# Optimization experiments

Hardware: AMD Instinct MI355X
Metric: run time of the kernel (lower is better)

## Reference

```python
import jax, jax.numpy as jnp
import numpy as np

B, MUL = 512, 64
DIMS = {0: 1, 1: 3, 2: 5}
PAIRS = [(0, 0), (0, 1), (0, 2), (1, 1), (1, 2), (2, 2)]  # l2 >= l1 (filter_symmetric)
LS_OUT = (0, 1, 2)


def _triples():
    for l1, l2 in PAIRS:
        for l3 in range(abs(l1 - l2), l1 + l2 + 1):
            if l3 in LS_OUT:
                yield (l1, l2, l3)


def setup_inputs() -> dict:
    key = jax.random.key(0)
    inp = {}
    for l in LS_OUT:
        key, k = jax.random.split(key)
        inp['x%d' % l] = jax.random.normal(k, (B, MUL, DIMS[l]), dtype=jnp.float32)
    for (l1, l2, l3) in _triples():
        key, k = jax.random.split(key)
        inp['w3j_%d_%d_%d' % (l1, l2, l3)] = jax.random.normal(
            k, (DIMS[l1], DIMS[l2], DIMS[l3]), dtype=jnp.float32) * 0.1
    return inp


def _forward(x, w):
    # ls_rule='full', channel_rule='full', filter_symmetric=True
    out = {l3: [] for l3 in LS_OUT}
    for l1, l2 in PAIRS:
        # outer product over channels and m-components: [B, i*j, 2l1+1, 2l2+1]
        op = jnp.einsum('bim,bjn->bijmn', x[l1], x[l2])
        b, i, j, m, n = op.shape
        op = op.reshape(b, i * j, m, n)
        for l3 in range(abs(l1 - l2), l1 + l2 + 1):
            if l3 in LS_OUT:
                # contract with Clebsch-Gordan / w3j coefficients
                out[l3].append(jnp.einsum('mnM,bimn->biM', w[(l1, l2, l3)], op))
    return tuple(jnp.concatenate(out[l3], axis=1) for l3 in LS_OUT)


def reference(x0, x1, x2,
              w3j_0_0_0, w3j_0_1_1, w3j_0_2_2,
              w3j_1_1_0, w3j_1_1_1, w3j_1_1_2,
              w3j_1_2_1, w3j_1_2_2,
              w3j_2_2_0, w3j_2_2_1, w3j_2_2_2):
    x = {0: x0, 1: x1, 2: x2}
    w = {(0, 0, 0): w3j_0_0_0, (0, 1, 1): w3j_0_1_1, (0, 2, 2): w3j_0_2_2,
         (1, 1, 0): w3j_1_1_0, (1, 1, 1): w3j_1_1_1, (1, 1, 2): w3j_1_1_2,
         (1, 2, 1): w3j_1_2_1, (1, 2, 2): w3j_1_2_2,
         (2, 2, 0): w3j_2_2_0, (2, 2, 1): w3j_2_2_1, (2, 2, 2): w3j_2_2_2}
    return _forward(x, w)
```

## Files before the change

kernel.cpp:

```cpp
#include <hip/hip_runtime.h>


#define OUT1_BASE (512 * 12288)
#define OUT2_BASE (OUT1_BASE + 512 * 49152)

#define WO_000 0
#define WO_011 1
#define WO_022 10
#define WO_110 35
#define WO_111 44
#define WO_112 71
#define WO_121 116
#define WO_122 161
#define WO_220 236
#define WO_221 261
#define WO_222 336
#define W_TOTAL 461

__global__ __launch_bounds__(256) void tp_kernel(
    const float* __restrict__ x0, const float* __restrict__ x1, const float* __restrict__ x2,
    const float* __restrict__ w000, const float* __restrict__ w011, const float* __restrict__ w022,
    const float* __restrict__ w110, const float* __restrict__ w111, const float* __restrict__ w112,
    const float* __restrict__ w121, const float* __restrict__ w122,
    const float* __restrict__ w220, const float* __restrict__ w221, const float* __restrict__ w222,
    float* __restrict__ out)
{
    __shared__ float s_x0[64];
    __shared__ float s_x1[192];
    __shared__ float s_x2[320];
    __shared__ float s_w[W_TOTAL];

    const int b    = blockIdx.x >> 4;
    const int tile = blockIdx.x & 15;
    const int t    = threadIdx.x;

    if (t < 64)  s_x0[t] = x0[b * 64 + t];
    if (t < 192) s_x1[t] = x1[b * 192 + t];
#pragma unroll
    for (int idx = t; idx < 320; idx += 256) s_x2[idx] = x2[b * 320 + idx];

    if (t < 1)   s_w[WO_000 + t] = w000[t];
    if (t < 9)   s_w[WO_011 + t] = w011[t];
    if (t < 25)  s_w[WO_022 + t] = w022[t];
    if (t < 9)   s_w[WO_110 + t] = w110[t];
    if (t < 27)  s_w[WO_111 + t] = w111[t];
    if (t < 45)  s_w[WO_112 + t] = w112[t];
    if (t < 45)  s_w[WO_121 + t] = w121[t];
    if (t < 75)  s_w[WO_122 + t] = w122[t];
    if (t < 25)  s_w[WO_220 + t] = w220[t];
    if (t < 75)  s_w[WO_221 + t] = w221[t];
    if (t < 125) s_w[WO_222 + t] = w222[t];

    __syncthreads();

    const int c = tile * 256 + t;
    const int i = c >> 6;
    const int j = c & 63;

    const float a0 = s_x0[i];
    const float b0 = s_x0[j];
    float a1m[3], b1n[3], a2m[5], b2n[5];
#pragma unroll
    for (int m = 0; m < 3; ++m) a1m[m] = s_x1[i * 3 + m];
#pragma unroll
    for (int n = 0; n < 3; ++n) b1n[n] = s_x1[j * 3 + n];
#pragma unroll
    for (int m = 0; m < 5; ++m) a2m[m] = s_x2[i * 5 + m];
#pragma unroll
    for (int n = 0; n < 5; ++n) b2n[n] = s_x2[j * 5 + n];

    float* __restrict__ out0 = out + (size_t)b * 12288;
    float* __restrict__ out1 = out + OUT1_BASE + (size_t)b * 49152;
    float* __restrict__ out2 = out + OUT2_BASE + (size_t)b * 81920;

    out0[c] = s_w[WO_000] * (a0 * b0);

    {
        float o[3] = {0.f, 0.f, 0.f};
#pragma unroll
        for (int n = 0; n < 3; ++n) {
            const float p = a0 * b1n[n];
#pragma unroll
            for (int M = 0; M < 3; ++M) o[M] += s_w[WO_011 + n * 3 + M] * p;
        }
        float* op = out1 + (size_t)c * 3;
#pragma unroll
        for (int M = 0; M < 3; ++M) op[M] = o[M];
    }

    {
        float o[5] = {0.f, 0.f, 0.f, 0.f, 0.f};
#pragma unroll
        for (int n = 0; n < 5; ++n) {
            const float p = a0 * b2n[n];
#pragma unroll
            for (int M = 0; M < 5; ++M) o[M] += s_w[WO_022 + n * 5 + M] * p;
        }
        float* op = out2 + (size_t)c * 5;
#pragma unroll
        for (int M = 0; M < 5; ++M) op[M] = o[M];
    }

    {
        float p[9];
#pragma unroll
        for (int m = 0; m < 3; ++m)
#pragma unroll
            for (int n = 0; n < 3; ++n) p[m * 3 + n] = a1m[m] * b1n[n];

        {
            float o = 0.f;
#pragma unroll
            for (int k = 0; k < 9; ++k) o += s_w[WO_110 + k] * p[k];
            out0[4096 + c] = o;
        }
        {
            float o[3] = {0.f, 0.f, 0.f};
#pragma unroll
            for (int k = 0; k < 9; ++k)
#pragma unroll
                for (int M = 0; M < 3; ++M) o[M] += s_w[WO_111 + k * 3 + M] * p[k];
            float* op = out1 + (size_t)(4096 + c) * 3;
#pragma unroll
            for (int M = 0; M < 3; ++M) op[M] = o[M];
        }
        {
            float o[5] = {0.f, 0.f, 0.f, 0.f, 0.f};
#pragma unroll
            for (int k = 0; k < 9; ++k)
#pragma unroll
                for (int M = 0; M < 5; ++M) o[M] += s_w[WO_112 + k * 5 + M] * p[k];
            float* op = out2 + (size_t)(4096 + c) * 5;
#pragma unroll
            for (int M = 0; M < 5; ++M) op[M] = o[M];
        }
    }

    {
        float p[15];
#pragma unroll
        for (int m = 0; m < 3; ++m)
#pragma unroll
            for (int n = 0; n < 5; ++n) p[m * 5 + n] = a1m[m] * b2n[n];

        {
            float o[3] = {0.f, 0.f, 0.f};
#pragma unroll
            for (int k = 0; k < 15; ++k)
#pragma unroll
                for (int M = 0; M < 3; ++M) o[M] += s_w[WO_121 + k * 3 + M] * p[k];
            float* op = out1 + (size_t)(2 * 4096 + c) * 3;
#pragma unroll
            for (int M = 0; M < 3; ++M) op[M] = o[M];
        }
        {
            float o[5] = {0.f, 0.f, 0.f, 0.f, 0.f};
#pragma unroll
            for (int k = 0; k < 15; ++k)
#pragma unroll
                for (int M = 0; M < 5; ++M) o[M] += s_w[WO_122 + k * 5 + M] * p[k];
            float* op = out2 + (size_t)(2 * 4096 + c) * 5;
#pragma unroll
            for (int M = 0; M < 5; ++M) op[M] = o[M];
        }
    }

    {
        float p[25];
#pragma unroll
        for (int m = 0; m < 5; ++m)
#pragma unroll
            for (int n = 0; n < 5; ++n) p[m * 5 + n] = a2m[m] * b2n[n];

        {
            float o = 0.f;
#pragma unroll
            for (int k = 0; k < 25; ++k) o += s_w[WO_220 + k] * p[k];
            out0[2 * 4096 + c] = o;
        }
        {
            float o[3] = {0.f, 0.f, 0.f};
#pragma unroll
            for (int k = 0; k < 25; ++k)
#pragma unroll
                for (int M = 0; M < 3; ++M) o[M] += s_w[WO_221 + k * 3 + M] * p[k];
            float* op = out1 + (size_t)(3 * 4096 + c) * 3;
#pragma unroll
            for (int M = 0; M < 3; ++M) op[M] = o[M];
        }
        {
            float o[5] = {0.f, 0.f, 0.f, 0.f, 0.f};
#pragma unroll
            for (int k = 0; k < 25; ++k)
#pragma unroll
                for (int M = 0; M < 5; ++M) o[M] += s_w[WO_222 + k * 5 + M] * p[k];
            float* op = out2 + (size_t)(3 * 4096 + c) * 5;
#pragma unroll
            for (int M = 0; M < 5; ++M) op[M] = o[M];
        }
    }
}

extern "C" void kernel_launch(void* const* d_in, const int* in_sizes, int n_in,
                              void* d_out, int out_size, void* d_ws, size_t ws_size,
                              hipStream_t stream) {
    const float* x0   = (const float*)d_in[0];
    const float* x1   = (const float*)d_in[1];
    const float* x2   = (const float*)d_in[2];
    const float* w000 = (const float*)d_in[3];
    const float* w011 = (const float*)d_in[4];
    const float* w022 = (const float*)d_in[5];
    const float* w110 = (const float*)d_in[6];
    const float* w111 = (const float*)d_in[7];
    const float* w112 = (const float*)d_in[8];
    const float* w121 = (const float*)d_in[9];
    const float* w122 = (const float*)d_in[10];
    const float* w220 = (const float*)d_in[11];
    const float* w221 = (const float*)d_in[12];
    const float* w222 = (const float*)d_in[13];
    float* outp = (float*)d_out;

    dim3 grid(512 * 16);
    dim3 block(256);
    tp_kernel<<<grid, block, 0, stream>>>(x0, x1, x2,
                                          w000, w011, w022, w110, w111, w112,
                                          w121, w122, w220, w221, w222, outp);
}
```

Measured before the change: 344.5 us.

## Stage l1/l2 outputs in shared memory and write them back as coalesced float4

Each thread now writes its stride-3 and stride-5 outputs for out1/out2 into a shared-memory tile. After a barrier, the block copies that tile to global memory with contiguous float4 stores, replacing the strided scalar stores that were poorly coalesced. The shared staging of inputs and weights is removed: x values and weights are now read straight from global memory, relying on cache broadcast. This raises LDS use to 32KB per block, which may lower occupancy, and adds a barrier.

```diff
diff --git a/kernel.cpp b/kernel.cpp
--- a/kernel.cpp
+++ b/kernel.cpp
@@ -3,19 +3,6 @@
 
 #define OUT1_BASE (512 * 12288)
 #define OUT2_BASE (OUT1_BASE + 512 * 49152)
-
-#define WO_000 0
-#define WO_011 1
-#define WO_022 10
-#define WO_110 35
-#define WO_111 44
-#define WO_112 71
-#define WO_121 116
-#define WO_122 161
-#define WO_220 236
-#define WO_221 261
-#define WO_222 336
-#define W_TOTAL 461
 
 __global__ __launch_bounds__(256) void tp_kernel(
     const float* __restrict__ x0, const float* __restrict__ x1, const float* __restrict__ x2,
@@ -25,179 +12,167 @@
     const float* __restrict__ w220, const float* __restrict__ w221, const float* __restrict__ w222,
     float* __restrict__ out)
 {
-    __shared__ float s_x0[64];
-    __shared__ float s_x1[192];
-    __shared__ float s_x2[320];
-    __shared__ float s_w[W_TOTAL];
+    __shared__ __align__(16) float s_out[8192];
 
     const int b    = blockIdx.x >> 4;
     const int tile = blockIdx.x & 15;
     const int t    = threadIdx.x;
-
-    if (t < 64)  s_x0[t] = x0[b * 64 + t];
-    if (t < 192) s_x1[t] = x1[b * 192 + t];
-#pragma unroll
-    for (int idx = t; idx < 320; idx += 256) s_x2[idx] = x2[b * 320 + idx];
-
-    if (t < 1)   s_w[WO_000 + t] = w000[t];
-    if (t < 9)   s_w[WO_011 + t] = w011[t];
-    if (t < 25)  s_w[WO_022 + t] = w022[t];
-    if (t < 9)   s_w[WO_110 + t] = w110[t];
-    if (t < 27)  s_w[WO_111 + t] = w111[t];
-    if (t < 45)  s_w[WO_112 + t] = w112[t];
-    if (t < 45)  s_w[WO_121 + t] = w121[t];
-    if (t < 75)  s_w[WO_122 + t] = w122[t];
-    if (t < 25)  s_w[WO_220 + t] = w220[t];
-    if (t < 75)  s_w[WO_221 + t] = w221[t];
-    if (t < 125) s_w[WO_222 + t] = w222[t];
+    const int c    = tile * 256 + t;
+    const int i    = c >> 6;
+    const int j    = c & 63;
+
+    const float a0 = x0[b * 64 + i];
+    const float b0 = x0[b * 64 + j];
+    float a1[3], b1[3], a2[5], b2[5];
+#pragma unroll
+    for (int m = 0; m < 3; ++m) a1[m] = x1[b * 192 + i * 3 + m];
+#pragma unroll
+    for (int n = 0; n < 3; ++n) b1[n] = x1[b * 192 + j * 3 + n];
+#pragma unroll
+    for (int m = 0; m < 5; ++m) a2[m] = x2[b * 320 + i * 5 + m];
+#pragma unroll
+    for (int n = 0; n < 5; ++n) b2[n] = x2[b * 320 + j * 5 + n];
+
+    float* __restrict__ out0 = out + (size_t)b * 12288;
+
+    out0[c] = w000[0] * (a0 * b0);
+
+    {
+        float o[3] = {0.f, 0.f, 0.f};
+#pragma unroll
+        for (int n = 0; n < 3; ++n) {
+            const float p = a0 * b1[n];
+#pragma unroll
+            for (int M = 0; M < 3; ++M) o[M] += w011[n * 3 + M] * p;
+        }
+#pragma unroll
+        for (int M = 0; M < 3; ++M) s_out[0 * 768 + t * 3 + M] = o[M];
+    }
+
+    {
+        float o[5] = {0.f, 0.f, 0.f, 0.f, 0.f};
+#pragma unroll
+        for (int n = 0; n < 5; ++n) {
+            const float p = a0 * b2[n];
+#pragma unroll
+            for (int M = 0; M < 5; ++M) o[M] += w022[n * 5 + M] * p;
+        }
+#pragma unroll
+        for (int M = 0; M < 5; ++M) s_out[3072 + 0 * 1280 + t * 5 + M] = o[M];
+    }
+
+    {
+        float p[9];
+#pragma unroll
+        for (int m = 0; m < 3; ++m)
+#pragma unroll
+            for (int n = 0; n < 3; ++n) p[m * 3 + n] = a1[m] * b1[n];
+
+        {
+            float o = 0.f;
+#pragma unroll
+            for (int k = 0; k < 9; ++k) o += w110[k] * p[k];
+            out0[4096 + c] = o;
+        }
+        {
+            float o[3] = {0.f, 0.f, 0.f};
+#pragma unroll
+            for (int k = 0; k < 9; ++k)
+#pragma unroll
+                for (int M = 0; M < 3; ++M) o[M] += w111[k * 3 + M] * p[k];
+#pragma unroll
+            for (int M = 0; M < 3; ++M) s_out[1 * 768 + t * 3 + M] = o[M];
+        }
+        {
+            float o[5] = {0.f, 0.f, 0.f, 0.f, 0.f};
+#pragma unroll
+            for (int k = 0; k < 9; ++k)
+#pragma unroll
+                for (int M = 0; M < 5; ++M) o[M] += w112[k * 5 + M] * p[k];
+#pragma unroll
+            for (int M = 0; M < 5; ++M) s_out[3072 + 1 * 1280 + t * 5 + M] = o[M];
+        }
+    }
+
+    {
+        float p[15];
+#pragma unroll
+        for (int m = 0; m < 3; ++m)
+#pragma unroll
+            for (int n = 0; n < 5; ++n) p[m * 5 + n] = a1[m] * b2[n];
+
+        {
+            float o[3] = {0.f, 0.f, 0.f};
+#pragma unroll
+            for (int k = 0; k < 15; ++k)
+#pragma unroll
+                for (int M = 0; M < 3; ++M) o[M] += w121[k * 3 + M] * p[k];
+#pragma unroll
+            for (int M = 0; M < 3; ++M) s_out[2 * 768 + t * 3 + M] = o[M];
+        }
+        {
+            float o[5] = {0.f, 0.f, 0.f, 0.f, 0.f};
+#pragma unroll
+            for (int k = 0; k < 15; ++k)
+#pragma unroll
+                for (int M = 0; M < 5; ++M) o[M] += w122[k * 5 + M] * p[k];
+#pragma unroll
+            for (int M = 0; M < 5; ++M) s_out[3072 + 2 * 1280 + t * 5 + M] = o[M];
+        }
+    }
+
+    {
+        float p[25];
+#pragma unroll
+        for (int m = 0; m < 5; ++m)
+#pragma unroll
+            for (int n = 0; n < 5; ++n) p[m * 5 + n] = a2[m] * b2[n];
+
+        {
+            float o = 0.f;
+#pragma unroll
+            for (int k = 0; k < 25; ++k) o += w220[k] * p[k];
+            out0[2 * 4096 + c] = o;
+        }
+        {
+            float o[3] = {0.f, 0.f, 0.f};
+#pragma unroll
+            for (int k = 0; k < 25; ++k)
+#pragma unroll
+                for (int M = 0; M < 3; ++M) o[M] += w221[k * 3 + M] * p[k];
+#pragma unroll
+            for (int M = 0; M < 3; ++M) s_out[3 * 768 + t * 3 + M] = o[M];
+        }
+        {
+            float o[5] = {0.f, 0.f, 0.f, 0.f, 0.f};
+#pragma unroll
+            for (int k = 0; k < 25; ++k)
+#pragma unroll
+                for (int M = 0; M < 5; ++M) o[M] += w222[k * 5 + M] * p[k];
+#pragma unroll
+            for (int M = 0; M < 5; ++M) s_out[3072 + 3 * 1280 + t * 5 + M] = o[M];
+        }
+    }
 
     __syncthreads();
 
-    const int c = tile * 256 + t;
-    const int i = c >> 6;
-    const int j = c & 63;
-
-    const float a0 = s_x0[i];
-    const float b0 = s_x0[j];
-    float a1m[3], b1n[3], a2m[5], b2n[5];
-#pragma unroll
-    for (int m = 0; m < 3; ++m) a1m[m] = s_x1[i * 3 + m];
-#pragma unroll
-    for (int n = 0; n < 3; ++n) b1n[n] = s_x1[j * 3 + n];
-#pragma unroll
-    for (int m = 0; m < 5; ++m) a2m[m] = s_x2[i * 5 + m];
-#pragma unroll
-    for (int n = 0; n < 5; ++n) b2n[n] = s_x2[j * 5 + n];
-
-    float* __restrict__ out0 = out + (size_t)b * 12288;
-    float* __restrict__ out1 = out + OUT1_BASE + (size_t)b * 49152;
-    float* __restrict__ out2 = out + OUT2_BASE + (size_t)b * 81920;
-
-    out0[c] = s_w[WO_000] * (a0 * b0);
-
-    {
-        float o[3] = {0.f, 0.f, 0.f};
-#pragma unroll
-        for (int n = 0; n < 3; ++n) {
-            const float p = a0 * b1n[n];
-#pragma unroll
-            for (int M = 0; M < 3; ++M) o[M] += s_w[WO_011 + n * 3 + M] * p;
-        }
-        float* op = out1 + (size_t)c * 3;
-#pragma unroll
-        for (int M = 0; M < 3; ++M) op[M] = o[M];
-    }
-
-    {
-        float o[5] = {0.f, 0.f, 0.f, 0.f, 0.f};
-#pragma unroll
-        for (int n = 0; n < 5; ++n) {
-            const float p = a0 * b2n[n];
-#pragma unroll
-            for (int M = 0; M < 5; ++M) o[M] += s_w[WO_022 + n * 5 + M] * p;
-        }
-        float* op = out2 + (size_t)c * 5;
-#pragma unroll
-        for (int M = 0; M < 5; ++M) op[M] = o[M];
-    }
-
-    {
-        float p[9];
-#pragma unroll
-        for (int m = 0; m < 3; ++m)
-#pragma unroll
-            for (int n = 0; n < 3; ++n) p[m * 3 + n] = a1m[m] * b1n[n];
-
-        {
-            float o = 0.f;
-#pragma unroll
-            for (int k = 0; k < 9; ++k) o += s_w[WO_110 + k] * p[k];
-            out0[4096 + c] = o;
-        }
-        {
-            float o[3] = {0.f, 0.f, 0.f};
-#pragma unroll
-            for (int k = 0; k < 9; ++k)
-#pragma unroll
-                for (int M = 0; M < 3; ++M) o[M] += s_w[WO_111 + k * 3 + M] * p[k];
-            float* op = out1 + (size_t)(4096 + c) * 3;
-#pragma unroll
-            for (int M = 0; M < 3; ++M) op[M] = o[M];
-        }
-        {
-            float o[5] = {0.f, 0.f, 0.f, 0.f, 0.f};
-#pragma unroll
-            for (int k = 0; k < 9; ++k)
-#pragma unroll
-                for (int M = 0; M < 5; ++M) o[M] += s_w[WO_112 + k * 5 + M] * p[k];
-            float* op = out2 + (size_t)(4096 + c) * 5;
-#pragma unroll
-            for (int M = 0; M < 5; ++M) op[M] = o[M];
-        }
-    }
-
-    {
-        float p[15];
-#pragma unroll
-        for (int m = 0; m < 3; ++m)
-#pragma unroll
-            for (int n = 0; n < 5; ++n) p[m * 5 + n] = a1m[m] * b2n[n];
-
-        {
-            float o[3] = {0.f, 0.f, 0.f};
-#pragma unroll
-            for (int k = 0; k < 15; ++k)
-#pragma unroll
-                for (int M = 0; M < 3; ++M) o[M] += s_w[WO_121 + k * 3 + M] * p[k];
-            float* op = out1 + (size_t)(2 * 4096 + c) * 3;
-#pragma unroll
-            for (int M = 0; M < 3; ++M) op[M] = o[M];
-        }
-        {
-            float o[5] = {0.f, 0.f, 0.f, 0.f, 0.f};
-#pragma unroll
-            for (int k = 0; k < 15; ++k)
-#pragma unroll
-                for (int M = 0; M < 5; ++M) o[M] += s_w[WO_122 + k * 5 + M] * p[k];
-            float* op = out2 + (size_t)(2 * 4096 + c) * 5;
-#pragma unroll
-            for (int M = 0; M < 5; ++M) op[M] = o[M];
-        }
-    }
-
-    {
-        float p[25];
-#pragma unroll
-        for (int m = 0; m < 5; ++m)
-#pragma unroll
-            for (int n = 0; n < 5; ++n) p[m * 5 + n] = a2m[m] * b2n[n];
-
-        {
-            float o = 0.f;
-#pragma unroll
-            for (int k = 0; k < 25; ++k) o += s_w[WO_220 + k] * p[k];
-            out0[2 * 4096 + c] = o;
-        }
-        {
-            float o[3] = {0.f, 0.f, 0.f};
-#pragma unroll
-            for (int k = 0; k < 25; ++k)
-#pragma unroll
-                for (int M = 0; M < 3; ++M) o[M] += s_w[WO_221 + k * 3 + M] * p[k];
-            float* op = out1 + (size_t)(3 * 4096 + c) * 3;
-#pragma unroll
-            for (int M = 0; M < 3; ++M) op[M] = o[M];
-        }
-        {
-            float o[5] = {0.f, 0.f, 0.f, 0.f, 0.f};
-#pragma unroll
-            for (int k = 0; k < 25; ++k)
-#pragma unroll
-                for (int M = 0; M < 5; ++M) o[M] += s_w[WO_222 + k * 5 + M] * p[k];
-            float* op = out2 + (size_t)(3 * 4096 + c) * 5;
-#pragma unroll
-            for (int M = 0; M < 5; ++M) op[M] = o[M];
-        }
+    const float4* __restrict__ s4 = (const float4*)s_out;
+#pragma unroll
+    for (int k = 0; k < 8; ++k) {
+        const int fi = k * 256 + t;
+        const float4 v = s4[fi];
+        int dst;
+        if (fi < 768) {
+            const int q   = fi / 192;
+            const int off = fi % 192;
+            dst = OUT1_BASE + b * 49152 + q * 12288 + tile * 768 + 4 * off;
+        } else {
+            const int r   = fi - 768;
+            const int q   = r / 320;
+            const int off = r % 320;
+            dst = OUT2_BASE + b * 81920 + q * 20480 + tile * 1280 + 4 * off;
+        }
+        *(float4*)(out + dst) = v;
     }
 }
 
```

Result: faster. 318.4 us (-7.6%).
